# Optimization experiments

Hardware: AMD Instinct MI355X
Metric: run time of the kernel (lower is better)

## Reference

```python
import jax, jax.numpy as jnp
import numpy as np

OUT_F = 8192
IN_F = 8192
RANK = 32
N_TOK = 128


def _pack_ternary(w_q):
    """Pack int8 ternary {-1,0,+1} [out,in] -> uint8 [out,in//4], LSB-first 2-bit codes."""
    enc = (w_q.astype(np.int32) + 1).astype(np.uint8).reshape(w_q.shape[0], -1, 4)
    packed = enc[:, :, 0] | (enc[:, :, 1] << 2) | (enc[:, :, 2] << 4) | (enc[:, :, 3] << 6)
    return packed


def setup_inputs() -> dict:
    key = jax.random.key(0)
    kx, kw, ks, ka, kb, kbias = jax.random.split(key, 6)
    x = jax.random.normal(kx, (N_TOK, IN_F), dtype=jnp.float32)
    # ternary weights in {-1,0,+1}
    w_q = np.asarray(jax.random.randint(kw, (OUT_F, IN_F), -1, 2, dtype=jnp.int32), dtype=np.int8)
    weight_packed = jnp.asarray(_pack_ternary(w_q), dtype=jnp.uint8)
    scale = jax.random.uniform(ks, (OUT_F,), dtype=jnp.float32, minval=0.01, maxval=0.05)
    lora_A = jax.random.normal(ka, (OUT_F, RANK), dtype=jnp.float32) * 0.02
    lora_B = jax.random.normal(kb, (RANK, IN_F), dtype=jnp.float32) * 0.02
    bias = jax.random.normal(kbias, (OUT_F,), dtype=jnp.float32) * 0.01
    return {"x": x, "weight_packed": weight_packed, "scale": scale,
            "lora_A": lora_A, "lora_B": lora_B, "bias": bias, "in_features": IN_F}


def _unpack_ternary(packed, in_features, dtype):
    # packed: uint8 [out, in//4]; LSB-first 2-bit codes, code-1 -> {-1,0,+1}
    p = packed.astype(jnp.int32)
    vals = jnp.stack([p & 3, (p >> 2) & 3, (p >> 4) & 3, (p >> 6) & 3], axis=-1)
    vals = vals.reshape(packed.shape[0], -1)[:, :in_features] - 1
    return vals.astype(dtype)


def reference(x, weight_packed, scale, lora_A, lora_B, bias, in_features):
    W = _unpack_ternary(weight_packed, in_features, x.dtype)  # [out, in]
    out = (x @ W.T) * scale[None, :]                          # [n, out]
    out = out + (x @ lora_B.T) @ lora_A.T                     # low-rank LoRA path
    out = out + bias
    return out
```

## Files before the change

kernel.cpp:

```cpp
#include <hip/hip_runtime.h>
#include <hip/hip_bf16.h>
#include <stdint.h>

typedef float f32x4 __attribute__((ext_vector_type(4)));
typedef __bf16 bf16x8 __attribute__((ext_vector_type(8)));
typedef unsigned short ushort8 __attribute__((ext_vector_type(8)));

#define N_TOK 128
#define OUT_F 8192
#define IN_F  8192
#define RANK  32

#define KSPLIT 8
#define KB    (IN_F / KSPLIT)
#define BK    64
#define NSTEP (KB / BK)
#define WSTRIDE 16
#define LKC   4

#define XB_OFF 0
#define TB_OFF ((size_t)N_TOK * IN_F * 2)
#define PO_OFF (TB_OFF + (size_t)LKC * N_TOK * RANK * 4)

__device__ __forceinline__ unsigned short bf16r(float f) {
    uint32_t u = __float_as_uint(f);
    return (unsigned short)((u + 0x7FFFu + ((u >> 16) & 1u)) >> 16);
}

__device__ __forceinline__ int swz(int row, int col) { return col ^ ((row & 7) << 3); }

__global__ __launch_bounds__(256) void cvt_x(const float* __restrict__ x,
                                             unsigned short* __restrict__ xt) {
    size_t f = (size_t)blockIdx.x * 256 + threadIdx.x;
    int lane = (int)(f & 63);
    int rec  = (int)(f >> 6);
    int ar16 = rec & 7;
    int kk   = (rec >> 3) & 1;
    int sblk = rec >> 4;
    int row = ar16 * 16 + (lane & 15);
    int k   = sblk * 64 + kk * 32 + (lane >> 4) * 8;
    const float4* sp = (const float4*)(x + (size_t)row * IN_F + k);
    float4 a = sp[0], b = sp[1];
    ushort8 o;
    o[0] = bf16r(a.x); o[1] = bf16r(a.y); o[2] = bf16r(a.z); o[3] = bf16r(a.w);
    o[4] = bf16r(b.x); o[5] = bf16r(b.y); o[6] = bf16r(b.z); o[7] = bf16r(b.w);
    *(ushort8*)(xt + f * 8) = o;
}

__global__ __launch_bounds__(256) void lora_t(const float* __restrict__ x,
                                              const float* __restrict__ lb,
                                              float* __restrict__ tB) {
    __shared__ float ts[256][33];
    __shared__ float ps[8][32];
    const int m = blockIdx.x >> 2, kc = blockIdx.x & 3;
    const int tid = threadIdx.x;
    const int c0 = kc * 2048 + tid * 8;
    float4 xv0 = *(const float4*)(x + (size_t)m * IN_F + c0);
    float4 xv1 = *(const float4*)(x + (size_t)m * IN_F + c0 + 4);
#pragma unroll
    for (int r = 0; r < RANK; ++r) {
        const float4* bp = (const float4*)(lb + (size_t)r * IN_F + c0);
        float4 b0 = bp[0], b1 = bp[1];
        float s = xv0.x * b0.x + xv0.y * b0.y + xv0.z * b0.z + xv0.w * b0.w +
                  xv1.x * b1.x + xv1.y * b1.y + xv1.z * b1.z + xv1.w * b1.w;
        ts[tid][r] = s;
    }
    __syncthreads();
    {
        int g = tid >> 5, r = tid & 31;
        float s = 0.f;
        for (int j = 0; j < 32; ++j) s += ts[g * 32 + j][r];
        ps[g][r] = s;
    }
    __syncthreads();
    if (tid < 32) {
        float s = 0.f;
#pragma unroll
        for (int g = 0; g < 8; ++g) s += ps[g][tid];
        tB[(kc * N_TOK + m) * RANK + tid] = s;
    }
}

__device__ __forceinline__ void decodeW(int4 v, uint32_t d[8]) {
    uint32_t p = (uint32_t)v.x | ((uint32_t)v.y << 8) |
                 ((uint32_t)v.z << 16) | ((uint32_t)v.w << 24);
    const uint32_t HI = 0x403F00BFu;
    const uint32_t LO = 0x00800080u;
#pragma unroll
    for (int j = 0; j < 8; ++j) {
        uint32_t c0 = (p >> (4 * j)) & 3u;
        uint32_t c1 = (p >> (4 * j + 2)) & 3u;
        uint32_t t = c0 | (c1 << 16);
        uint32_t sel = (t | (t << 8)) + 0x04000400u;
        d[j] = __builtin_amdgcn_perm(HI, LO, sel);
    }
}

__global__ __launch_bounds__(256) void ternary_gemm(const unsigned short* __restrict__ xt,
                                                    const int* __restrict__ wp,
                                                    unsigned short* __restrict__ pO) {
    __shared__ unsigned short ww[128][64];
    const int tid = threadIdx.x;
    const int nb = blockIdx.x >> 3;
    const int ks = blockIdx.x & 7;
    const int n0 = nb * 128;
    const int lane = tid & 63;
    const int wid = tid >> 6;
    const int wr = wid >> 1, wc = wid & 1;

    const int srow = tid >> 2;
    const int xcol = (tid & 3) * 16;
    const int* pg0 = wp + (size_t)(n0 + srow) * (IN_F / 4) + ks * (KB / 4) + (tid & 3) * 4;
    const int* pg1 = pg0 + (size_t)64 * (IN_F / 4);

    const int arow = lane & 15;
    const int kgrp = (lane >> 4) * 8;
    const int wc0 = swz(srow, xcol), wc1 = swz(srow, xcol + 8);

    const unsigned short* abase = xt + ((size_t)(ks * NSTEP) * 16) * 512 + lane * 8;
#define LDA(s_, kk_, ar_) \
    (*(const bf16x8*)(abase + ((size_t)((s_)*16 + (kk_)*8 + (wr * 4 + (ar_)))) * 512))

    f32x4 acc[4][4];
#pragma unroll
    for (int i = 0; i < 4; ++i)
#pragma unroll
        for (int j = 0; j < 4; ++j) acc[i][j] = (f32x4){0.f, 0.f, 0.f, 0.f};

    bf16x8 aX[4][2], aY[4][2];
    int4 wP[2][2];

#pragma unroll
    for (int ar = 0; ar < 4; ++ar) {
        aX[ar][0] = LDA(0, 0, ar);
        aX[ar][1] = LDA(0, 1, ar);
    }
    wP[0][0] = *(const int4*)(pg0);
    wP[0][1] = *(const int4*)(pg1);
    wP[1][0] = *(const int4*)(pg0 + WSTRIDE);
    wP[1][1] = *(const int4*)(pg1 + WSTRIDE);
    {
        uint32_t d0[8], d1[8];
        decodeW(wP[0][0], d0);
        decodeW(wP[0][1], d1);
        *(uint4*)&ww[srow][wc0]      = make_uint4(d0[0], d0[1], d0[2], d0[3]);
        *(uint4*)&ww[srow][wc1]      = make_uint4(d0[4], d0[5], d0[6], d0[7]);
        *(uint4*)&ww[srow + 64][wc0] = make_uint4(d1[0], d1[1], d1[2], d1[3]);
        *(uint4*)&ww[srow + 64][wc1] = make_uint4(d1[4], d1[5], d1[6], d1[7]);
    }
    wP[0][0] = *(const int4*)(pg0 + 2 * WSTRIDE);
    wP[0][1] = *(const int4*)(pg1 + 2 * WSTRIDE);
    __builtin_amdgcn_sched_barrier(0);
    asm volatile("s_waitcnt lgkmcnt(0)" ::: "memory");
    __builtin_amdgcn_s_barrier();
    __builtin_amdgcn_sched_barrier(0);

#pragma unroll
    for (int s = 0; s < NSTEP; ++s) {
        bf16x8 (*aCur)[2] = (s & 1) ? aY : aX;
        bf16x8 (*aNxt)[2] = (s & 1) ? aX : aY;
        bf16x8 bfr[2][4];
#pragma unroll
        for (int kk = 0; kk < 2; ++kk)
#pragma unroll
            for (int br = 0; br < 4; ++br) {
                int row = wc * 64 + br * 16 + arow;
                bfr[kk][br] = *(const bf16x8*)&ww[row][swz(row, kk * 32 + kgrp)];
            }
#pragma unroll
        for (int ar = 0; ar < 4; ++ar) {
#pragma unroll
            for (int kk = 0; kk < 2; ++kk)
#pragma unroll
                for (int br = 0; br < 4; ++br)
                    acc[ar][br] = __builtin_amdgcn_mfma_f32_16x16x32_bf16(
                        aCur[ar][kk], bfr[kk][br], acc[ar][br], 0, 0, 0);
            if (s + 1 < NSTEP) {
                aNxt[ar][0] = LDA(s + 1, 0, ar);
                aNxt[ar][1] = LDA(s + 1, 1, ar);
            }
        }
        if (s + 1 < NSTEP) {
            uint32_t d0[8], d1[8];
            decodeW(wP[(s + 1) & 1][0], d0);
            decodeW(wP[(s + 1) & 1][1], d1);
            __builtin_amdgcn_sched_barrier(0);
            __builtin_amdgcn_s_barrier();
            __builtin_amdgcn_sched_barrier(0);
            *(uint4*)&ww[srow][wc0]      = make_uint4(d0[0], d0[1], d0[2], d0[3]);
            *(uint4*)&ww[srow][wc1]      = make_uint4(d0[4], d0[5], d0[6], d0[7]);
            *(uint4*)&ww[srow + 64][wc0] = make_uint4(d1[0], d1[1], d1[2], d1[3]);
            *(uint4*)&ww[srow + 64][wc1] = make_uint4(d1[4], d1[5], d1[6], d1[7]);
            if (s + 2 < NSTEP) {
                wP[s & 1][0] = *(const int4*)(pg0 + (s + 2) * WSTRIDE);
                wP[s & 1][1] = *(const int4*)(pg1 + (s + 2) * WSTRIDE);
            }
            __builtin_amdgcn_sched_barrier(0);
            asm volatile("s_waitcnt lgkmcnt(0)" ::: "memory");
            __builtin_amdgcn_s_barrier();
            __builtin_amdgcn_sched_barrier(0);
        }
    }
#undef LDA

    unsigned short* po = pO + ((size_t)ks << 20);
    const int mrow = (lane >> 4) * 4;
#pragma unroll
    for (int ar = 0; ar < 4; ++ar) {
#pragma unroll
        for (int br = 0; br < 4; ++br) {
            int m = wr * 64 + ar * 16 + mrow;
            int n = n0 + wc * 64 + br * 16 + arow;
            unsigned short* pp = po + (size_t)m * OUT_F + n;
#pragma unroll
            for (int j = 0; j < 4; ++j) pp[(size_t)j * OUT_F] = bf16r(acc[ar][br][j]);
        }
    }
}

__global__ __launch_bounds__(256) void reduce_out(const unsigned short* __restrict__ pO,
                                                  const float* __restrict__ tB,
                                                  const float* __restrict__ scale,
                                                  const float* __restrict__ lora_A,
                                                  const float* __restrict__ bias,
                                                  float* __restrict__ out) {
    __shared__ float ts[4][RANK];
    int nb = blockIdx.x & 15, mg = blockIdx.x >> 4;
    int tid = threadIdx.x;
    int m0 = mg * 4;
    if (tid < 128) {
        int i = tid >> 5, r = tid & 31;
        float s = 0.f;
#pragma unroll
        for (int c = 0; c < LKC; ++c) s += tB[(c * N_TOK + m0 + i) * RANK + r];
        ts[i][r] = s;
    }
    __syncthreads();
    int n = nb * 512 + tid * 2;
    float sc0 = scale[n], sc1 = scale[n + 1];
    float bs0 = bias[n], bs1 = bias[n + 1];
    float4 a0[8], a1[8];
    const float4* ap0 = (const float4*)(lora_A + (size_t)n * RANK);
    const float4* ap1 = (const float4*)(lora_A + (size_t)(n + 1) * RANK);
#pragma unroll
    for (int q = 0; q < 8; ++q) { a0[q] = ap0[q]; a1[q] = ap1[q]; }
#pragma unroll
    for (int i = 0; i < 4; ++i) {
        int m = m0 + i;
        const unsigned short* pp = pO + (size_t)m * OUT_F + n;
        float s0 = 0.f, s1 = 0.f;
#pragma unroll
        for (int c = 0; c < KSPLIT; ++c) {
            uint32_t u = *(const uint32_t*)(pp + ((size_t)c << 20));
            s0 += __uint_as_float(u << 16);
            s1 += __uint_as_float(u & 0xFFFF0000u);
        }
        float l0 = 0.f, l1 = 0.f;
#pragma unroll
        for (int q = 0; q < 8; ++q) {
            float4 tv = *(const float4*)&ts[i][q * 4];
            l0 = fmaf(tv.x, a0[q].x, l0); l0 = fmaf(tv.y, a0[q].y, l0);
            l0 = fmaf(tv.z, a0[q].z, l0); l0 = fmaf(tv.w, a0[q].w, l0);
            l1 = fmaf(tv.x, a1[q].x, l1); l1 = fmaf(tv.y, a1[q].y, l1);
            l1 = fmaf(tv.z, a1[q].z, l1); l1 = fmaf(tv.w, a1[q].w, l1);
        }
        out[(size_t)m * OUT_F + n]     = fmaf(s0, sc0, l0 + bs0);
        out[(size_t)m * OUT_F + n + 1] = fmaf(s1, sc1, l1 + bs1);
    }
}

extern "C" void kernel_launch(void* const* d_in, const int* in_sizes, int n_in,
                              void* d_out, int out_size, void* d_ws, size_t ws_size,
                              hipStream_t stream) {
    const float* x      = (const float*)d_in[0];
    const int*   wp     = (const int*)d_in[1];
    const float* scale  = (const float*)d_in[2];
    const float* lora_A = (const float*)d_in[3];
    const float* lora_B = (const float*)d_in[4];
    const float* bias   = (const float*)d_in[5];
    float* out = (float*)d_out;

    char* ws = (char*)d_ws;
    unsigned short* xt = (unsigned short*)(ws + XB_OFF);
    float* tB = (float*)(ws + TB_OFF);
    unsigned short* pO = (unsigned short*)(ws + PO_OFF);

    cvt_x<<<512, 256, 0, stream>>>(x, xt);
    lora_t<<<N_TOK * LKC, 256, 0, stream>>>(x, lora_B, tB);
    ternary_gemm<<<(OUT_F / 128) * KSPLIT, 256, 0, stream>>>(xt, wp, pO);
    reduce_out<<<16 * 32, 256, 0, stream>>>(pO, tB, scale, lora_A, bias, out);
}
```

Baseline: 49.61 us.

## Decode ternary weights straight into MFMA registers, drop LDS staging, double K-split

The GEMM no longer stages decoded weights through shared memory with barriers. Each lane now loads its own packed bytes for its B fragments, double-buffered two steps ahead, and decodes them in registers right before the MFMAs. The K-split doubles from 8 to 16 to launch more blocks and hide load latency. In exchange, the two row-waves that share a column each decode the same weights, and the partial-output buffer and its reduction traffic double. This also relies on the workspace and reduction kernel being sized for 16 splits.

```diff
diff --git a/kernel.cpp b/kernel.cpp
--- a/kernel.cpp
+++ b/kernel.cpp
@@ -5,17 +5,17 @@
 typedef float f32x4 __attribute__((ext_vector_type(4)));
 typedef __bf16 bf16x8 __attribute__((ext_vector_type(8)));
 typedef unsigned short ushort8 __attribute__((ext_vector_type(8)));
+typedef uint32_t u32x4 __attribute__((ext_vector_type(4)));
 
 #define N_TOK 128
 #define OUT_F 8192
 #define IN_F  8192
 #define RANK  32
 
-#define KSPLIT 8
+#define KSPLIT 16
 #define KB    (IN_F / KSPLIT)
 #define BK    64
 #define NSTEP (KB / BK)
-#define WSTRIDE 16
 #define LKC   4
 
 #define XB_OFF 0
@@ -26,8 +26,6 @@
     uint32_t u = __float_as_uint(f);
     return (unsigned short)((u + 0x7FFFu + ((u >> 16) & 1u)) >> 16);
 }
-
-__device__ __forceinline__ int swz(int row, int col) { return col ^ ((row & 7) << 3); }
 
 __global__ __launch_bounds__(256) void cvt_x(const float* __restrict__ x,
                                              unsigned short* __restrict__ xt) {
@@ -81,130 +79,91 @@
     }
 }
 
-__device__ __forceinline__ void decodeW(int4 v, uint32_t d[8]) {
-    uint32_t p = (uint32_t)v.x | ((uint32_t)v.y << 8) |
-                 ((uint32_t)v.z << 16) | ((uint32_t)v.w << 24);
+__device__ __forceinline__ bf16x8 decode8(int2 v) {
+    uint32_t p = (uint32_t)(v.x & 0xFF) | (((uint32_t)(v.y & 0xFF)) << 8);
     const uint32_t HI = 0x403F00BFu;
     const uint32_t LO = 0x00800080u;
-#pragma unroll
-    for (int j = 0; j < 8; ++j) {
+    u32x4 d;
+#pragma unroll
+    for (int j = 0; j < 4; ++j) {
         uint32_t c0 = (p >> (4 * j)) & 3u;
         uint32_t c1 = (p >> (4 * j + 2)) & 3u;
         uint32_t t = c0 | (c1 << 16);
         uint32_t sel = (t | (t << 8)) + 0x04000400u;
         d[j] = __builtin_amdgcn_perm(HI, LO, sel);
     }
+    return __builtin_bit_cast(bf16x8, d);
 }
 
 __global__ __launch_bounds__(256) void ternary_gemm(const unsigned short* __restrict__ xt,
                                                     const int* __restrict__ wp,
                                                     unsigned short* __restrict__ pO) {
-    __shared__ unsigned short ww[128][64];
     const int tid = threadIdx.x;
-    const int nb = blockIdx.x >> 3;
-    const int ks = blockIdx.x & 7;
+    const int nb = blockIdx.x >> 4;
+    const int ks = blockIdx.x & 15;
     const int n0 = nb * 128;
     const int lane = tid & 63;
     const int wid = tid >> 6;
     const int wr = wid >> 1, wc = wid & 1;
-
-    const int srow = tid >> 2;
-    const int xcol = (tid & 3) * 16;
-    const int* pg0 = wp + (size_t)(n0 + srow) * (IN_F / 4) + ks * (KB / 4) + (tid & 3) * 4;
-    const int* pg1 = pg0 + (size_t)64 * (IN_F / 4);
-
     const int arow = lane & 15;
-    const int kgrp = (lane >> 4) * 8;
-    const int wc0 = swz(srow, xcol), wc1 = swz(srow, xcol + 8);
+    const int kq = lane >> 4;
 
     const unsigned short* abase = xt + ((size_t)(ks * NSTEP) * 16) * 512 + lane * 8;
 #define LDA(s_, kk_, ar_) \
     (*(const bf16x8*)(abase + ((size_t)((s_)*16 + (kk_)*8 + (wr * 4 + (ar_)))) * 512))
 
+    const int* wrow = wp + (size_t)(n0 + wc * 64 + arow) * (IN_F / 4) + ks * (KB / 4) + kq * 2;
+#define LDW(s_, br_, kk_) (*(const int2*)(wrow + (br_)*16*2048 + (s_)*16 + (kk_)*8))
+
     f32x4 acc[4][4];
 #pragma unroll
     for (int i = 0; i < 4; ++i)
 #pragma unroll
         for (int j = 0; j < 4; ++j) acc[i][j] = (f32x4){0.f, 0.f, 0.f, 0.f};
 
-    bf16x8 aX[4][2], aY[4][2];
-    int4 wP[2][2];
-
-#pragma unroll
-    for (int ar = 0; ar < 4; ++ar) {
-        aX[ar][0] = LDA(0, 0, ar);
-        aX[ar][1] = LDA(0, 1, ar);
-    }
-    wP[0][0] = *(const int4*)(pg0);
-    wP[0][1] = *(const int4*)(pg1);
-    wP[1][0] = *(const int4*)(pg0 + WSTRIDE);
-    wP[1][1] = *(const int4*)(pg1 + WSTRIDE);
-    {
-        uint32_t d0[8], d1[8];
-        decodeW(wP[0][0], d0);
-        decodeW(wP[0][1], d1);
-        *(uint4*)&ww[srow][wc0]      = make_uint4(d0[0], d0[1], d0[2], d0[3]);
-        *(uint4*)&ww[srow][wc1]      = make_uint4(d0[4], d0[5], d0[6], d0[7]);
-        *(uint4*)&ww[srow + 64][wc0] = make_uint4(d1[0], d1[1], d1[2], d1[3]);
-        *(uint4*)&ww[srow + 64][wc1] = make_uint4(d1[4], d1[5], d1[6], d1[7]);
-    }
-    wP[0][0] = *(const int4*)(pg0 + 2 * WSTRIDE);
-    wP[0][1] = *(const int4*)(pg1 + 2 * WSTRIDE);
-    __builtin_amdgcn_sched_barrier(0);
-    asm volatile("s_waitcnt lgkmcnt(0)" ::: "memory");
-    __builtin_amdgcn_s_barrier();
-    __builtin_amdgcn_sched_barrier(0);
+    int2 wbA[4][2], wbB[4][2];
+
+#pragma unroll
+    for (int br = 0; br < 4; ++br) {
+        wbA[br][0] = LDW(0, br, 0);
+        wbA[br][1] = LDW(0, br, 1);
+    }
+#pragma unroll
+    for (int br = 0; br < 4; ++br) {
+        wbB[br][0] = LDW(1, br, 0);
+        wbB[br][1] = LDW(1, br, 1);
+    }
 
 #pragma unroll
     for (int s = 0; s < NSTEP; ++s) {
-        bf16x8 (*aCur)[2] = (s & 1) ? aY : aX;
-        bf16x8 (*aNxt)[2] = (s & 1) ? aX : aY;
-        bf16x8 bfr[2][4];
-#pragma unroll
-        for (int kk = 0; kk < 2; ++kk)
+        int2 (*wcur)[2] = (s & 1) ? wbB : wbA;
+#pragma unroll
+        for (int kk = 0; kk < 2; ++kk) {
+            bf16x8 aK[4];
+#pragma unroll
+            for (int ar = 0; ar < 4; ++ar) aK[ar] = LDA(s, kk, ar);
 #pragma unroll
             for (int br = 0; br < 4; ++br) {
-                int row = wc * 64 + br * 16 + arow;
-                bfr[kk][br] = *(const bf16x8*)&ww[row][swz(row, kk * 32 + kgrp)];
+                bf16x8 b = decode8(wcur[br][kk]);
+#pragma unroll
+                for (int ar = 0; ar < 4; ++ar)
+                    acc[ar][br] = __builtin_amdgcn_mfma_f32_16x16x32_bf16(
+                        aK[ar], b, acc[ar][br], 0, 0, 0);
             }
-#pragma unroll
-        for (int ar = 0; ar < 4; ++ar) {
-#pragma unroll
-            for (int kk = 0; kk < 2; ++kk)
-#pragma unroll
-                for (int br = 0; br < 4; ++br)
-                    acc[ar][br] = __builtin_amdgcn_mfma_f32_16x16x32_bf16(
-                        aCur[ar][kk], bfr[kk][br], acc[ar][br], 0, 0, 0);
-            if (s + 1 < NSTEP) {
-                aNxt[ar][0] = LDA(s + 1, 0, ar);
-                aNxt[ar][1] = LDA(s + 1, 1, ar);
+        }
+        if (s + 2 < NSTEP) {
+#pragma unroll
+            for (int br = 0; br < 4; ++br) {
+                wcur[br][0] = LDW(s + 2, br, 0);
+                wcur[br][1] = LDW(s + 2, br, 1);
             }
         }
-        if (s + 1 < NSTEP) {
-            uint32_t d0[8], d1[8];
-            decodeW(wP[(s + 1) & 1][0], d0);
-            decodeW(wP[(s + 1) & 1][1], d1);
-            __builtin_amdgcn_sched_barrier(0);
-            __builtin_amdgcn_s_barrier();
-            __builtin_amdgcn_sched_barrier(0);
-            *(uint4*)&ww[srow][wc0]      = make_uint4(d0[0], d0[1], d0[2], d0[3]);
-            *(uint4*)&ww[srow][wc1]      = make_uint4(d0[4], d0[5], d0[6], d0[7]);
-            *(uint4*)&ww[srow + 64][wc0] = make_uint4(d1[0], d1[1], d1[2], d1[3]);
-            *(uint4*)&ww[srow + 64][wc1] = make_uint4(d1[4], d1[5], d1[6], d1[7]);
-            if (s + 2 < NSTEP) {
-                wP[s & 1][0] = *(const int4*)(pg0 + (s + 2) * WSTRIDE);
-                wP[s & 1][1] = *(const int4*)(pg1 + (s + 2) * WSTRIDE);
-            }
-            __builtin_amdgcn_sched_barrier(0);
-            asm volatile("s_waitcnt lgkmcnt(0)" ::: "memory");
-            __builtin_amdgcn_s_barrier();
-            __builtin_amdgcn_sched_barrier(0);
-        }
     }
 #undef LDA
+#undef LDW
 
     unsigned short* po = pO + ((size_t)ks << 20);
-    const int mrow = (lane >> 4) * 4;
+    const int mrow = kq * 4;
 #pragma unroll
     for (int ar = 0; ar < 4; ++ar) {
 #pragma unroll
```

After: 84.64 us. 70.6% more time.

## Double-buffer decoded weight tile in LDS and double split-K to sixteen

Applied to the files above, without the earlier changes.

The decoded ternary weight tile now has two shared-memory buffers, so the next step's tile is written while the current one is read, which removes one block barrier per K-step. The weight prefetch distance grows to three steps. Activation fragments are now loaded per k-slice inside the step rather than held in a register double-buffer, and the kernel requests three blocks per CU through launch bounds. Split-K goes from 8 to 16 to put more blocks on the GPU, at the cost of twice as many partial outputs to write and reduce, and of more exposed global-load latency on the activation operands.

```diff
diff --git a/kernel.cpp b/kernel.cpp
--- a/kernel.cpp
+++ b/kernel.cpp
@@ -11,7 +11,7 @@
 #define IN_F  8192
 #define RANK  32
 
-#define KSPLIT 8
+#define KSPLIT 16
 #define KB    (IN_F / KSPLIT)
 #define BK    64
 #define NSTEP (KB / BK)
@@ -96,13 +96,13 @@
     }
 }
 
-__global__ __launch_bounds__(256) void ternary_gemm(const unsigned short* __restrict__ xt,
-                                                    const int* __restrict__ wp,
-                                                    unsigned short* __restrict__ pO) {
-    __shared__ unsigned short ww[128][64];
+__global__ __launch_bounds__(256, 3) void ternary_gemm(const unsigned short* __restrict__ xt,
+                                                       const int* __restrict__ wp,
+                                                       unsigned short* __restrict__ pO) {
+    __shared__ unsigned short ww[2][128][64];
     const int tid = threadIdx.x;
-    const int nb = blockIdx.x >> 3;
-    const int ks = blockIdx.x & 7;
+    const int nb = blockIdx.x >> 4;
+    const int ks = blockIdx.x & 15;
     const int n0 = nb * 128;
     const int lane = tid & 63;
     const int wid = tid >> 6;
@@ -127,14 +127,8 @@
 #pragma unroll
         for (int j = 0; j < 4; ++j) acc[i][j] = (f32x4){0.f, 0.f, 0.f, 0.f};
 
-    bf16x8 aX[4][2], aY[4][2];
     int4 wP[2][2];
 
-#pragma unroll
-    for (int ar = 0; ar < 4; ++ar) {
-        aX[ar][0] = LDA(0, 0, ar);
-        aX[ar][1] = LDA(0, 1, ar);
-    }
     wP[0][0] = *(const int4*)(pg0);
     wP[0][1] = *(const int4*)(pg1);
     wP[1][0] = *(const int4*)(pg0 + WSTRIDE);
@@ -143,10 +137,10 @@
         uint32_t d0[8], d1[8];
         decodeW(wP[0][0], d0);
         decodeW(wP[0][1], d1);
-        *(uint4*)&ww[srow][wc0]      = make_uint4(d0[0], d0[1], d0[2], d0[3]);
-        *(uint4*)&ww[srow][wc1]      = make_uint4(d0[4], d0[5], d0[6], d0[7]);
-        *(uint4*)&ww[srow + 64][wc0] = make_uint4(d1[0], d1[1], d1[2], d1[3]);
-        *(uint4*)&ww[srow + 64][wc1] = make_uint4(d1[4], d1[5], d1[6], d1[7]);
+        *(uint4*)&ww[0][srow][wc0]      = make_uint4(d0[0], d0[1], d0[2], d0[3]);
+        *(uint4*)&ww[0][srow][wc1]      = make_uint4(d0[4], d0[5], d0[6], d0[7]);
+        *(uint4*)&ww[0][srow + 64][wc0] = make_uint4(d1[0], d1[1], d1[2], d1[3]);
+        *(uint4*)&ww[0][srow + 64][wc1] = make_uint4(d1[4], d1[5], d1[6], d1[7]);
     }
     wP[0][0] = *(const int4*)(pg0 + 2 * WSTRIDE);
     wP[0][1] = *(const int4*)(pg1 + 2 * WSTRIDE);
@@ -157,43 +151,35 @@
 
 #pragma unroll
     for (int s = 0; s < NSTEP; ++s) {
-        bf16x8 (*aCur)[2] = (s & 1) ? aY : aX;
-        bf16x8 (*aNxt)[2] = (s & 1) ? aX : aY;
-        bf16x8 bfr[2][4];
-#pragma unroll
-        for (int kk = 0; kk < 2; ++kk)
+        const int cur = s & 1, nxt = cur ^ 1;
+#pragma unroll
+        for (int kk = 0; kk < 2; ++kk) {
+            bf16x8 aK[4], bfr[4];
+#pragma unroll
+            for (int ar = 0; ar < 4; ++ar) aK[ar] = LDA(s, kk, ar);
 #pragma unroll
             for (int br = 0; br < 4; ++br) {
                 int row = wc * 64 + br * 16 + arow;
-                bfr[kk][br] = *(const bf16x8*)&ww[row][swz(row, kk * 32 + kgrp)];
+                bfr[br] = *(const bf16x8*)&ww[cur][row][swz(row, kk * 32 + kgrp)];
             }
 #pragma unroll
-        for (int ar = 0; ar < 4; ++ar) {
-#pragma unroll
-            for (int kk = 0; kk < 2; ++kk)
+            for (int ar = 0; ar < 4; ++ar)
 #pragma unroll
                 for (int br = 0; br < 4; ++br)
                     acc[ar][br] = __builtin_amdgcn_mfma_f32_16x16x32_bf16(
-                        aCur[ar][kk], bfr[kk][br], acc[ar][br], 0, 0, 0);
-            if (s + 1 < NSTEP) {
-                aNxt[ar][0] = LDA(s + 1, 0, ar);
-                aNxt[ar][1] = LDA(s + 1, 1, ar);
-            }
+                        aK[ar], bfr[br], acc[ar][br], 0, 0, 0);
         }
         if (s + 1 < NSTEP) {
             uint32_t d0[8], d1[8];
-            decodeW(wP[(s + 1) & 1][0], d0);
-            decodeW(wP[(s + 1) & 1][1], d1);
-            __builtin_amdgcn_sched_barrier(0);
-            __builtin_amdgcn_s_barrier();
-            __builtin_amdgcn_sched_barrier(0);
-            *(uint4*)&ww[srow][wc0]      = make_uint4(d0[0], d0[1], d0[2], d0[3]);
-            *(uint4*)&ww[srow][wc1]      = make_uint4(d0[4], d0[5], d0[6], d0[7]);
-            *(uint4*)&ww[srow + 64][wc0] = make_uint4(d1[0], d1[1], d1[2], d1[3]);
-            *(uint4*)&ww[srow + 64][wc1] = make_uint4(d1[4], d1[5], d1[6], d1[7]);
-            if (s + 2 < NSTEP) {
-                wP[s & 1][0] = *(const int4*)(pg0 + (s + 2) * WSTRIDE);
-                wP[s & 1][1] = *(const int4*)(pg1 + (s + 2) * WSTRIDE);
+            decodeW(wP[nxt][0], d0);
+            decodeW(wP[nxt][1], d1);
+            *(uint4*)&ww[nxt][srow][wc0]      = make_uint4(d0[0], d0[1], d0[2], d0[3]);
+            *(uint4*)&ww[nxt][srow][wc1]      = make_uint4(d0[4], d0[5], d0[6], d0[7]);
+            *(uint4*)&ww[nxt][srow + 64][wc0] = make_uint4(d1[0], d1[1], d1[2], d1[3]);
+            *(uint4*)&ww[nxt][srow + 64][wc1] = make_uint4(d1[4], d1[5], d1[6], d1[7]);
+            if (s + 3 < NSTEP) {
+                wP[nxt][0] = *(const int4*)(pg0 + (s + 3) * WSTRIDE);
+                wP[nxt][1] = *(const int4*)(pg1 + (s + 3) * WSTRIDE);
             }
             __builtin_amdgcn_sched_barrier(0);
             asm volatile("s_waitcnt lgkmcnt(0)" ::: "memory");
```

Measured after the change: 56.16 us. 13.2% more time.
